# Kernel optimization log

Hardware: AMD Instinct MI355X
Metric: run time of the kernel (lower is better)

Reference implementation:

```python
import jax, jax.numpy as jnp
import numpy as np

B, OUT, IN = 4096, 1024, 1024
BN_EPS = 1e-5


def setup_inputs() -> dict:
    key = jax.random.key(0)
    kx, k1, k2, k3 = jax.random.split(key, 4)
    # kaiming_uniform_ with a=sqrt(5): bound = sqrt(6 / ((1+a^2) * fan_in)) = 1/sqrt(fan_in)
    bound = 1.0 / np.sqrt(IN)
    x = jax.random.normal(kx, (B, IN), dtype=jnp.float32)
    c1 = jax.random.uniform(k1, (OUT, IN), jnp.float32, -bound, bound)
    c2 = jax.random.uniform(k2, (OUT, IN), jnp.float32, -bound, bound)
    c3 = jax.random.uniform(k3, (OUT, IN), jnp.float32, -bound, bound)
    bias = jnp.zeros((OUT, IN), jnp.float32)
    gamma = jnp.ones((OUT,), jnp.float32)   # BatchNorm1d weight
    beta = jnp.zeros((OUT,), jnp.float32)   # BatchNorm1d bias
    return {"x": x, "c1": c1, "c2": c2, "c3": c3, "bias": bias,
            "gamma": gamma, "beta": beta}


def reference(x, c1, c2, c3, bias, gamma, beta):
    # Fused polynomial 'matmul': out[b,o] = sum_i x*c1 + x^2*c2 + x^3*c3 + bias
    x2 = x * x
    x3 = x2 * x
    y = (jnp.einsum('bi,oi->bo', x, c1)
         + jnp.einsum('bi,oi->bo', x2, c2)
         + jnp.einsum('bi,oi->bo', x3, c3)
         + jnp.sum(bias, axis=1))  # bias reduced over in_features
    # BatchNorm1d (training mode: batch statistics, biased variance)
    mean = jnp.mean(y, axis=0)
    var = jnp.var(y, axis=0)
    return (y - mean) * jax.lax.rsqrt(var + BN_EPS) * gamma + beta
```

## Files before the change

kernel.cpp:

```cpp
#include <hip/hip_runtime.h>
#include <stdint.h>

#define B_ROWS 4096
#define OUTF   1024
#define INF    1024
#define KTOT   3072
#define BN_EPS 1e-5f
#define BM 128
#define BN 128
#define BK 64
#define NSTEP (KTOT / BK)

typedef short  short8  __attribute__((ext_vector_type(8)));
typedef float  floatx4 __attribute__((ext_vector_type(4)));

struct alignas(8) s4 { short x, y, z, w; };

#define WAIT_VM4 0x0F74
#define WAIT_VM2 0x0F72
#define WAIT_VM0 0x0F70

__device__ __forceinline__ short f2bf(float f) {
  union { float f; uint32_t u; } cv; cv.f = f;
  uint32_t u = cv.u;
  uint32_t r = (u + 0x7fffu + ((u >> 16) & 1u)) >> 16;
  return (short)r;
}

__device__ __forceinline__ void load_lds16(const void* g, void* l) {
  __builtin_amdgcn_global_load_lds(
      (const __attribute__((address_space(1))) uint32_t*)(uintptr_t)g,
      (__attribute__((address_space(3))) uint32_t*)(uint32_t)(uintptr_t)l,
      16, 0, 0);
}

__global__ void prep_all(const float4* __restrict__ x4,
                         const float4* __restrict__ c1, const float4* __restrict__ c2,
                         const float4* __restrict__ c3,
                         short* __restrict__ Xb, short* __restrict__ Wb) {
  int b = blockIdx.x;
  if (b < 4096) {
    int idx = b * 256 + threadIdx.x;
    float4 v = x4[idx];
    int row = idx >> 8;
    int c   = (idx & 255) << 2;
    size_t base = (size_t)row * KTOT + c;
    s4 p1 = { f2bf(v.x), f2bf(v.y), f2bf(v.z), f2bf(v.w) };
    float ax = v.x * v.x, ay = v.y * v.y, az = v.z * v.z, aw = v.w * v.w;
    s4 p2 = { f2bf(ax), f2bf(ay), f2bf(az), f2bf(aw) };
    s4 p3 = { f2bf(ax * v.x), f2bf(ay * v.y), f2bf(az * v.z), f2bf(aw * v.w) };
    *(s4*)&Xb[base]        = p1;
    *(s4*)&Xb[base + 1024] = p2;
    *(s4*)&Xb[base + 2048] = p3;
  } else {
    int idx = (b - 4096) * 256 + threadIdx.x;
    int row = idx >> 8;
    int c   = (idx & 255) << 2;
    size_t base = (size_t)row * KTOT + c;
    float4 a = c1[idx], bb = c2[idx], d = c3[idx];
    s4 p1 = { f2bf(a.x),  f2bf(a.y),  f2bf(a.z),  f2bf(a.w)  };
    s4 p2 = { f2bf(bb.x), f2bf(bb.y), f2bf(bb.z), f2bf(bb.w) };
    s4 p3 = { f2bf(d.x),  f2bf(d.y),  f2bf(d.z),  f2bf(d.w)  };
    *(s4*)&Wb[base]        = p1;
    *(s4*)&Wb[base + 1024] = p2;
    *(s4*)&Wb[base + 2048] = p3;
  }
}

__global__ __launch_bounds__(1024, 4) void gemm_poly(
    const short* __restrict__ Xb, const short* __restrict__ Wb,
    float* __restrict__ Y, float* __restrict__ psum, float* __restrict__ psq) {
  __shared__ __align__(16) short As[4][BM * BK];
  __shared__ __align__(16) short Bs[4][BN * BK];
  const int tid  = threadIdx.x;
  const int lane = tid & 63;
  const int wave = tid >> 6;
  const int wr = wave >> 2;
  const int wc = wave & 3;
  const int lb  = blockIdx.x;
  const int xcd = lb & 7;
  const int sl  = lb >> 3;
  const int bx  = sl & 7;
  const int by  = xcd * 4 + (sl >> 3);
  const int row0 = by * BM;
  const int col0 = bx * BN;
  const short* Ag = Xb + (size_t)row0 * KTOT;
  const short* Bg = Wb + (size_t)col0 * KTOT;
  const int frag_m = lane & 15;
  const int sel = lane >> 4;
  floatx4 acc[2][2] = {};

  const int soff = (tid >> 3) * KTOT + ((tid & 7) ^ ((tid >> 3) & 7)) * 8;
  const int ldst = tid * 8;

  #pragma unroll
  for (int t = 0; t < 3; ++t) {
    load_lds16(Ag + soff + t * BK, &As[t][ldst]);
    load_lds16(Bg + soff + t * BK, &Bs[t][ldst]);
  }

#define GSTEP(CUR, PRE, KT_PRE, DO_PRE, WAITIMM)                              \
  {                                                                           \
    __builtin_amdgcn_s_waitcnt(WAITIMM);                                      \
    __builtin_amdgcn_s_barrier();                                             \
    if (DO_PRE) {                                                             \
      load_lds16(Ag + soff + (KT_PRE), &As[PRE][ldst]);                       \
      load_lds16(Bg + soff + (KT_PRE), &Bs[PRE][ldst]);                       \
    }                                                                         \
    _Pragma("unroll")                                                         \
    for (int s = 0; s < 2; ++s) {                                             \
      short8 af[2], bfr[2];                                                   \
      _Pragma("unroll")                                                       \
      for (int i = 0; i < 2; ++i) {                                           \
        int r = wr * 32 + i * 16 + frag_m;                                    \
        int p = (s * 4 + sel) ^ (r & 7);                                      \
        af[i] = *(const short8*)&As[CUR][r * BK + p * 8];                     \
      }                                                                       \
      _Pragma("unroll")                                                       \
      for (int j = 0; j < 2; ++j) {                                           \
        int r = wc * 32 + j * 16 + frag_m;                                    \
        int p = (s * 4 + sel) ^ (r & 7);                                      \
        bfr[j] = *(const short8*)&Bs[CUR][r * BK + p * 8];                    \
      }                                                                       \
      _Pragma("unroll")                                                       \
      for (int i = 0; i < 2; ++i)                                             \
        _Pragma("unroll")                                                     \
        for (int j = 0; j < 2; ++j)                                           \
          acc[i][j] = __builtin_amdgcn_mfma_f32_16x16x32_bf16(                \
              af[i], bfr[j], acc[i][j], 0, 0, 0);                             \
    }                                                                         \
  }

  for (int t4 = 0; t4 < 44; t4 += 4) {
    GSTEP(0, 3, (t4 + 3) * BK, 1, WAIT_VM4);
    GSTEP(1, 0, (t4 + 4) * BK, 1, WAIT_VM4);
    GSTEP(2, 1, (t4 + 5) * BK, 1, WAIT_VM4);
    GSTEP(3, 2, (t4 + 6) * BK, 1, WAIT_VM4);
  }
  GSTEP(0, 3, 47 * BK, 1, WAIT_VM4);
  GSTEP(1, 0, 0, 0, WAIT_VM4);
  GSTEP(2, 0, 0, 0, WAIT_VM2);
  GSTEP(3, 0, 0, 0, WAIT_VM0);
#undef GSTEP

  float* colred = (float*)&As[0][0];
  float sv[2] = {0.f, 0.f}, sq[2] = {0.f, 0.f};
  #pragma unroll
  for (int j = 0; j < 2; ++j)
    #pragma unroll
    for (int i = 0; i < 2; ++i)
      #pragma unroll
      for (int r = 0; r < 4; ++r) {
        float v = acc[i][j][r];
        sv[j] += v; sq[j] += v * v;
      }
  #pragma unroll
  for (int j = 0; j < 2; ++j) {
    sv[j] += __shfl_xor(sv[j], 16, 64); sv[j] += __shfl_xor(sv[j], 32, 64);
    sq[j] += __shfl_xor(sq[j], 16, 64); sq[j] += __shfl_xor(sq[j], 32, 64);
  }
  if (sel == 0) {
    #pragma unroll
    for (int j = 0; j < 2; ++j) {
      int cc = wc * 32 + j * 16 + frag_m;
      colred[(wr * 2 + 0) * 128 + cc] = sv[j];
      colred[(wr * 2 + 1) * 128 + cc] = sq[j];
    }
  }
  #pragma unroll
  for (int j = 0; j < 2; ++j) {
    int gc = col0 + wc * 32 + j * 16 + frag_m;
    #pragma unroll
    for (int i = 0; i < 2; ++i) {
      int gr = row0 + wr * 32 + i * 16 + sel * 4;
      #pragma unroll
      for (int r = 0; r < 4; ++r)
        Y[(size_t)(gr + r) * OUTF + gc] = acc[i][j][r];
    }
  }
  __syncthreads();
  if (tid < BN) {
    float s0 = colred[0 * 128 + tid] + colred[2 * 128 + tid]
             + colred[4 * 128 + tid] + colred[6 * 128 + tid];
    float s1 = colred[1 * 128 + tid] + colred[3 * 128 + tid]
             + colred[5 * 128 + tid] + colred[7 * 128 + tid];
    psum[(size_t)by * OUTF + col0 + tid] = s0;
    psq [(size_t)by * OUTF + col0 + tid] = s1;
  }
}

__global__ void bn_fused(const float* __restrict__ psum, const float* __restrict__ psq,
                         const float* __restrict__ gamma, const float* __restrict__ beta,
                         float* __restrict__ Y) {
  __shared__ float sc[32], sh[32];
  const int c0 = blockIdx.x * 32;
  const int t = threadIdx.x;
  if (t < 32) {
    float s = 0.f, s2 = 0.f;
    #pragma unroll 8
    for (int p = 0; p < 32; ++p) {
      s  += psum[p * OUTF + c0 + t];
      s2 += psq [p * OUTF + c0 + t];
    }
    float mean = s * (1.0f / B_ROWS);
    float var  = s2 * (1.0f / B_ROWS) - mean * mean;
    float scale = gamma[c0 + t] * rsqrtf(var + BN_EPS);
    sc[t] = scale;
    sh[t] = beta[c0 + t] - mean * scale;
  }
  __syncthreads();
  const int f4c = t & 7;
  const int rr  = t >> 3;
  const int row0 = blockIdx.y * 256;
  float4* Y4 = (float4*)Y;
  const int cb = f4c * 4;
  float s0 = sc[cb], s1 = sc[cb+1], s2 = sc[cb+2], s3 = sc[cb+3];
  float h0 = sh[cb], h1 = sh[cb+1], h2 = sh[cb+2], h3 = sh[cb+3];
  #pragma unroll
  for (int it = 0; it < 8; ++it) {
    int row = row0 + it * 32 + rr;
    size_t idx = (size_t)row * 256 + (c0 >> 2) + f4c;
    float4 v = Y4[idx];
    v.x = v.x * s0 + h0; v.y = v.y * s1 + h1;
    v.z = v.z * s2 + h2; v.w = v.w * s3 + h3;
    Y4[idx] = v;
  }
}

extern "C" void kernel_launch(void* const* d_in, const int* in_sizes, int n_in,
                              void* d_out, int out_size, void* d_ws, size_t ws_size,
                              hipStream_t stream) {
  const float* x     = (const float*)d_in[0];
  const float* c1    = (const float*)d_in[1];
  const float* c2    = (const float*)d_in[2];
  const float* c3    = (const float*)d_in[3];
  const float* gamma = (const float*)d_in[5];
  const float* beta  = (const float*)d_in[6];
  float* out = (float*)d_out;
  char* ws = (char*)d_ws;

  short* Xb   = (short*)(ws);
  short* Wb   = (short*)(ws + 25165824);
  float* psum = (float*)(ws + 31457280);
  float* psq  = (float*)(ws + 31588352);

  prep_all<<<5120, 256, 0, stream>>>((const float4*)x, (const float4*)c1,
                                     (const float4*)c2, (const float4*)c3,
                                     Xb, Wb);

  gemm_poly<<<256, 1024, 0, stream>>>(Xb, Wb, out, psum, psq);

  dim3 bgrid(OUTF / 32, B_ROWS / 256);
  bn_fused<<<bgrid, 256, 0, stream>>>(psum, psq, gamma, beta, out);
}
```

Baseline: 124.1 us.

## Split GEMM K dimension in two and combine partials in separate stats kernel

The polynomial GEMM now uses split-K: 512 blocks of 512 threads each compute half of the K=3072 reduction with BK=32 and a 4x2 MFMA tile per wave, writing two partial outputs. A new combine_stats kernel sums the partials and computes per-column sums and squares, and bn_apply re-reads both partials to produce the normalized output. This raises the block count to fill more CUs, at the cost of two extra full-size fp32 buffers in memory traffic and an additional kernel launch.

Result: slower. 135.7 us (+9.4%).

```diff
diff --git a/kernel.cpp b/kernel.cpp
--- a/kernel.cpp
+++ b/kernel.cpp
@@ -5,11 +5,12 @@
 #define OUTF   1024
 #define INF    1024
 #define KTOT   3072
+#define KHALF  1536
 #define BN_EPS 1e-5f
 #define BM 128
 #define BN 128
-#define BK 64
-#define NSTEP (KTOT / BK)
+#define BK 32
+#define NSTEP (KHALF / BK)
 
 typedef short  short8  __attribute__((ext_vector_type(8)));
 typedef float  floatx4 __attribute__((ext_vector_type(4)));
@@ -67,9 +68,9 @@
   }
 }
 
-__global__ __launch_bounds__(1024, 4) void gemm_poly(
+__global__ __launch_bounds__(512, 4) void gemm_poly(
     const short* __restrict__ Xb, const short* __restrict__ Wb,
-    float* __restrict__ Y, float* __restrict__ psum, float* __restrict__ psq) {
+    float* __restrict__ P0, float* __restrict__ P1) {
   __shared__ __align__(16) short As[4][BM * BK];
   __shared__ __align__(16) short Bs[4][BN * BK];
   const int tid  = threadIdx.x;
@@ -77,20 +78,24 @@
   const int wave = tid >> 6;
   const int wr = wave >> 2;
   const int wc = wave & 3;
-  const int lb  = blockIdx.x;
-  const int xcd = lb & 7;
-  const int sl  = lb >> 3;
-  const int bx  = sl & 7;
-  const int by  = xcd * 4 + (sl >> 3);
+  const int lb   = blockIdx.x;
+  const int xcd  = lb & 7;
+  const int rest = lb >> 3;
+  const int kp   = rest & 1;
+  const int sl   = rest >> 1;
+  const int bx   = sl & 7;
+  const int by   = xcd * 4 + (sl >> 3);
   const int row0 = by * BM;
   const int col0 = bx * BN;
-  const short* Ag = Xb + (size_t)row0 * KTOT;
-  const short* Bg = Wb + (size_t)col0 * KTOT;
+  const short* Ag = Xb + (size_t)row0 * KTOT + kp * KHALF;
+  const short* Bg = Wb + (size_t)col0 * KTOT + kp * KHALF;
   const int frag_m = lane & 15;
   const int sel = lane >> 4;
-  floatx4 acc[2][2] = {};
-
-  const int soff = (tid >> 3) * KTOT + ((tid & 7) ^ ((tid >> 3) & 7)) * 8;
+  floatx4 acc[4][2] = {};
+
+  const int Rr = tid >> 3, qq = tid & 7;
+  const int ls = qq ^ (Rr & 7);
+  const int soff = (Rr * 2 + (ls >> 2)) * KTOT + (ls & 3) * 8;
   const int ldst = tid * 8;
 
   #pragma unroll
@@ -107,28 +112,25 @@
       load_lds16(Ag + soff + (KT_PRE), &As[PRE][ldst]);                       \
       load_lds16(Bg + soff + (KT_PRE), &Bs[PRE][ldst]);                       \
     }                                                                         \
+    short8 af[4], bfr[2];                                                     \
     _Pragma("unroll")                                                         \
-    for (int s = 0; s < 2; ++s) {                                             \
-      short8 af[2], bfr[2];                                                   \
+    for (int i = 0; i < 4; ++i) {                                             \
+      int r = wr * 64 + i * 16 + frag_m;                                      \
+      int q = (((r & 1) << 2) | sel) ^ ((r >> 1) & 7);                        \
+      af[i] = *(const short8*)&As[CUR][(r >> 1) * 64 + q * 8];                \
+    }                                                                         \
+    _Pragma("unroll")                                                         \
+    for (int j = 0; j < 2; ++j) {                                             \
+      int r = wc * 32 + j * 16 + frag_m;                                      \
+      int q = (((r & 1) << 2) | sel) ^ ((r >> 1) & 7);                        \
+      bfr[j] = *(const short8*)&Bs[CUR][(r >> 1) * 64 + q * 8];               \
+    }                                                                         \
+    _Pragma("unroll")                                                         \
+    for (int i = 0; i < 4; ++i)                                               \
       _Pragma("unroll")                                                       \
-      for (int i = 0; i < 2; ++i) {                                           \
-        int r = wr * 32 + i * 16 + frag_m;                                    \
-        int p = (s * 4 + sel) ^ (r & 7);                                      \
-        af[i] = *(const short8*)&As[CUR][r * BK + p * 8];                     \
-      }                                                                       \
-      _Pragma("unroll")                                                       \
-      for (int j = 0; j < 2; ++j) {                                           \
-        int r = wc * 32 + j * 16 + frag_m;                                    \
-        int p = (s * 4 + sel) ^ (r & 7);                                      \
-        bfr[j] = *(const short8*)&Bs[CUR][r * BK + p * 8];                    \
-      }                                                                       \
-      _Pragma("unroll")                                                       \
-      for (int i = 0; i < 2; ++i)                                             \
-        _Pragma("unroll")                                                     \
-        for (int j = 0; j < 2; ++j)                                           \
-          acc[i][j] = __builtin_amdgcn_mfma_f32_16x16x32_bf16(                \
-              af[i], bfr[j], acc[i][j], 0, 0, 0);                             \
-    }                                                                         \
+      for (int j = 0; j < 2; ++j)                                             \
+        acc[i][j] = __builtin_amdgcn_mfma_f32_16x16x32_bf16(                  \
+            af[i], bfr[j], acc[i][j], 0, 0, 0);                               \
   }
 
   for (int t4 = 0; t4 < 44; t4 += 4) {
@@ -143,86 +145,85 @@
   GSTEP(3, 0, 0, 0, WAIT_VM0);
 #undef GSTEP
 
-  float* colred = (float*)&As[0][0];
-  float sv[2] = {0.f, 0.f}, sq[2] = {0.f, 0.f};
-  #pragma unroll
-  for (int j = 0; j < 2; ++j)
-    #pragma unroll
-    for (int i = 0; i < 2; ++i)
-      #pragma unroll
-      for (int r = 0; r < 4; ++r) {
-        float v = acc[i][j][r];
-        sv[j] += v; sq[j] += v * v;
-      }
-  #pragma unroll
-  for (int j = 0; j < 2; ++j) {
-    sv[j] += __shfl_xor(sv[j], 16, 64); sv[j] += __shfl_xor(sv[j], 32, 64);
-    sq[j] += __shfl_xor(sq[j], 16, 64); sq[j] += __shfl_xor(sq[j], 32, 64);
-  }
-  if (sel == 0) {
-    #pragma unroll
-    for (int j = 0; j < 2; ++j) {
-      int cc = wc * 32 + j * 16 + frag_m;
-      colred[(wr * 2 + 0) * 128 + cc] = sv[j];
-      colred[(wr * 2 + 1) * 128 + cc] = sq[j];
-    }
-  }
+  float* Pw = kp ? P1 : P0;
   #pragma unroll
   for (int j = 0; j < 2; ++j) {
     int gc = col0 + wc * 32 + j * 16 + frag_m;
     #pragma unroll
-    for (int i = 0; i < 2; ++i) {
-      int gr = row0 + wr * 32 + i * 16 + sel * 4;
+    for (int i = 0; i < 4; ++i) {
+      int gr = row0 + wr * 64 + i * 16 + sel * 4;
       #pragma unroll
       for (int r = 0; r < 4; ++r)
-        Y[(size_t)(gr + r) * OUTF + gc] = acc[i][j][r];
+        Pw[(size_t)(gr + r) * OUTF + gc] = acc[i][j][r];
     }
   }
+}
+
+__global__ void combine_stats(const float4* __restrict__ P0,
+                              const float4* __restrict__ P1,
+                              float* __restrict__ psum, float* __restrict__ psq) {
+  __shared__ float red[2][8][4][32];
+  const int t = threadIdx.x;
+  const int f4c = t & 7, rr = t >> 3;
+  const int cx = blockIdx.x, ry = blockIdx.y;
+  float s[4] = {0,0,0,0}, s2[4] = {0,0,0,0};
+  #pragma unroll
+  for (int it = 0; it < 8; ++it) {
+    int row = ry * 256 + it * 32 + rr;
+    size_t idx = (size_t)row * 256 + cx * 8 + f4c;
+    float4 a = P0[idx], b = P1[idx];
+    float y0 = a.x + b.x, y1 = a.y + b.y, y2 = a.z + b.z, y3 = a.w + b.w;
+    s[0] += y0; s[1] += y1; s[2] += y2; s[3] += y3;
+    s2[0] += y0*y0; s2[1] += y1*y1; s2[2] += y2*y2; s2[3] += y3*y3;
+  }
+  #pragma unroll
+  for (int k = 0; k < 4; ++k) { red[0][f4c][k][rr] = s[k]; red[1][f4c][k][rr] = s2[k]; }
   __syncthreads();
-  if (tid < BN) {
-    float s0 = colred[0 * 128 + tid] + colred[2 * 128 + tid]
-             + colred[4 * 128 + tid] + colred[6 * 128 + tid];
-    float s1 = colred[1 * 128 + tid] + colred[3 * 128 + tid]
-             + colred[5 * 128 + tid] + colred[7 * 128 + tid];
-    psum[(size_t)by * OUTF + col0 + tid] = s0;
-    psq [(size_t)by * OUTF + col0 + tid] = s1;
-  }
-}
-
-__global__ void bn_fused(const float* __restrict__ psum, const float* __restrict__ psq,
+  if (t < 32) {
+    float S = 0.f, SQ = 0.f;
+    #pragma unroll 8
+    for (int r = 0; r < 32; ++r) { S += red[0][t >> 2][t & 3][r]; SQ += red[1][t >> 2][t & 3][r]; }
+    psum[ry * OUTF + cx * 32 + t] = S;
+    psq [ry * OUTF + cx * 32 + t] = SQ;
+  }
+}
+
+__global__ void bn_apply(const float4* __restrict__ P0, const float4* __restrict__ P1,
+                         const float* __restrict__ psum, const float* __restrict__ psq,
                          const float* __restrict__ gamma, const float* __restrict__ beta,
                          float* __restrict__ Y) {
   __shared__ float sc[32], sh[32];
-  const int c0 = blockIdx.x * 32;
+  const int cx = blockIdx.x, ry = blockIdx.y;
   const int t = threadIdx.x;
   if (t < 32) {
     float s = 0.f, s2 = 0.f;
-    #pragma unroll 8
-    for (int p = 0; p < 32; ++p) {
-      s  += psum[p * OUTF + c0 + t];
-      s2 += psq [p * OUTF + c0 + t];
+    #pragma unroll
+    for (int p = 0; p < 16; ++p) {
+      s  += psum[p * OUTF + cx * 32 + t];
+      s2 += psq [p * OUTF + cx * 32 + t];
     }
     float mean = s * (1.0f / B_ROWS);
     float var  = s2 * (1.0f / B_ROWS) - mean * mean;
-    float scale = gamma[c0 + t] * rsqrtf(var + BN_EPS);
+    float scale = gamma[cx * 32 + t] * rsqrtf(var + BN_EPS);
     sc[t] = scale;
-    sh[t] = beta[c0 + t] - mean * scale;
+    sh[t] = beta[cx * 32 + t] - mean * scale;
   }
   __syncthreads();
-  const int f4c = t & 7;
-  const int rr  = t >> 3;
-  const int row0 = blockIdx.y * 256;
-  float4* Y4 = (float4*)Y;
+  const int f4c = t & 7, rr = t >> 3;
   const int cb = f4c * 4;
   float s0 = sc[cb], s1 = sc[cb+1], s2 = sc[cb+2], s3 = sc[cb+3];
   float h0 = sh[cb], h1 = sh[cb+1], h2 = sh[cb+2], h3 = sh[cb+3];
+  float4* Y4 = (float4*)Y;
   #pragma unroll
   for (int it = 0; it < 8; ++it) {
-    int row = row0 + it * 32 + rr;
-    size_t idx = (size_t)row * 256 + (c0 >> 2) + f4c;
-    float4 v = Y4[idx];
-    v.x = v.x * s0 + h0; v.y = v.y * s1 + h1;
-    v.z = v.z * s2 + h2; v.w = v.w * s3 + h3;
+    int row = ry * 256 + it * 32 + rr;
+    size_t idx = (size_t)row * 256 + cx * 8 + f4c;
+    float4 a = P0[idx], b = P1[idx];
+    float4 v;
+    v.x = (a.x + b.x) * s0 + h0;
+    v.y = (a.y + b.y) * s1 + h1;
+    v.z = (a.z + b.z) * s2 + h2;
+    v.w = (a.w + b.w) * s3 + h3;
     Y4[idx] = v;
   }
 }
@@ -241,15 +242,20 @@
 
   short* Xb   = (short*)(ws);
   short* Wb   = (short*)(ws + 25165824);
-  float* psum = (float*)(ws + 31457280);
-  float* psq  = (float*)(ws + 31588352);
+  float* P0   = (float*)(ws + 31457280);
+  float* P1   = (float*)(ws + 48234496);
+  float* psum = (float*)(ws + 65011712);
+  float* psq  = (float*)(ws + 65077248);
 
   prep_all<<<5120, 256, 0, stream>>>((const float4*)x, (const float4*)c1,
                                      (const float4*)c2, (const float4*)c3,
                                      Xb, Wb);
 
-  gemm_poly<<<256, 1024, 0, stream>>>(Xb, Wb, out, psum, psq);
-
-  dim3 bgrid(OUTF / 32, B_ROWS / 256);
-  bn_fused<<<bgrid, 256, 0, stream>>>(psum, psq, gamma, beta, out);
-}
+  gemm_poly<<<512, 512, 0, stream>>>(Xb, Wb, P0, P1);
+
+  dim3 sgrid(32, 16);
+  combine_stats<<<sgrid, 256, 0, stream>>>((const float4*)P0, (const float4*)P1,
+                                           psum, psq);
+  bn_apply<<<sgrid, 256, 0, stream>>>((const float4*)P0, (const float4*)P1,
+                                      psum, psq, gamma, beta, out);
+}
```
